# Performance work log

Measured on AMD Instinct MI355X. Metric: run time of the kernel, lower is better.

## Reference

```python
import jax, jax.numpy as jnp
import numpy as np

D = 1024
H = 16
T = D // H  # head dim; attention() scales by sqrt(Q.size(2)) == sqrt(T)
B = 4
S = 2048


def setup_inputs() -> dict:
    key = jax.random.key(0)
    ks = jax.random.split(key, 11)
    lim = 1.0 / np.sqrt(D)  # nn.Linear default init range
    inp = {
        "Q": jax.random.normal(ks[0], (B, S, D), jnp.float32),
        "K": jax.random.normal(ks[1], (B, S, D), jnp.float32),
        "V": jax.random.normal(ks[2], (B, S, D), jnp.float32),
        # per-head Q/K/V projections, stacked: weight [h, t, d], bias [h, t]
        "Wq": jax.random.uniform(ks[3], (H, T, D), jnp.float32, -lim, lim),
        "bq": jax.random.uniform(ks[4], (H, T), jnp.float32, -lim, lim),
        "Wk": jax.random.uniform(ks[5], (H, T, D), jnp.float32, -lim, lim),
        "bk": jax.random.uniform(ks[6], (H, T), jnp.float32, -lim, lim),
        "Wv": jax.random.uniform(ks[7], (H, T, D), jnp.float32, -lim, lim),
        "bv": jax.random.uniform(ks[8], (H, T), jnp.float32, -lim, lim),
        # output projection d -> d
        "Wo": jax.random.uniform(ks[9], (D, D), jnp.float32, -lim, lim),
        "bo": jax.random.uniform(ks[10], (D,), jnp.float32, -lim, lim),
    }
    return inp


def reference(Q, K, V, Wq, bq, Wk, bk, Wv, bv, Wo, bo):
    # Per-head projections, batched over heads: [b, h, s, t]
    q = jnp.einsum("bsd,htd->bhst", Q, Wq) + bq[None, :, None, :]
    k = jnp.einsum("bsd,htd->bhst", K, Wk) + bk[None, :, None, :]
    v = jnp.einsum("bsd,htd->bhst", V, Wv) + bv[None, :, None, :]
    # scaled dot-product attention; scale uses head dim T (Q.size(2) in source)
    scores = jnp.einsum("bhqt,bhkt->bhqk", q, k) / jnp.sqrt(jnp.asarray(T, q.dtype))
    probs = jax.nn.softmax(scores, axis=-1)
    ctx = jnp.einsum("bhqk,bhkt->bhqt", probs, v)
    # concat heads along feature dim (head i -> slice [i*t:(i+1)*t])
    z = ctx.transpose(0, 2, 1, 3).reshape(B, S, D)
    return jnp.einsum("bsd,ed->bse", z, Wo) + bo
```

## Files before the change

### kernel.cpp

```cpp
#include <hip/hip_runtime.h>

typedef unsigned short u16;
typedef unsigned int u32;
typedef __bf16 bf16x8 __attribute__((ext_vector_type(8)));
typedef __bf16 bf16x2 __attribute__((ext_vector_type(2)));
typedef float f32x4 __attribute__((ext_vector_type(4)));
typedef float f32x16 __attribute__((ext_vector_type(16)));
typedef unsigned int u32x2v __attribute__((ext_vector_type(2)));

#define BB 4
#define SS 2048
#define DD 1024
#define HH 16
#define TT 64

#define QSCALE 0.18033688011112042f

__device__ __forceinline__ u16 f32_to_bf16(float f) {
    unsigned int u = __float_as_uint(f);
    u += 0x7fffu + ((u >> 16) & 1u);
    return (u16)(u >> 16);
}

__device__ __forceinline__ u32 pack_bf16x2(float a, float b) {
    bf16x2 t;
    t[0] = (__bf16)a;
    t[1] = (__bf16)b;
    return __builtin_bit_cast(u32, t);
}

__device__ __forceinline__ void pswap(u32& x, u32& y) {
#if __has_builtin(__builtin_amdgcn_permlane32_swap)
    u32x2v r = __builtin_amdgcn_permlane32_swap(x, y, false, false);
    x = r[0];
    y = r[1];
#else
    u32 sx = __shfl_xor(y, 32);
    u32 sy = __shfl_xor(x, 32);
    bool lo = (threadIdx.x & 32) == 0;
    u32 nx = lo ? x : sx;
    u32 ny = lo ? sy : y;
    x = nx;
    y = ny;
#endif
}

#define GLDS(g, l) __builtin_amdgcn_global_load_lds(                              \
    (const __attribute__((address_space(1))) void*)(g),                            \
    (__attribute__((address_space(3))) void*)(l), 16, 0, 0)

struct PackArgs {
    const float* s[4];
    u16* d[4];
};

__global__ __launch_bounds__(256) void pack_multi(PackArgs a) {
    const float* __restrict__ src = a.s[blockIdx.y];
    u16* __restrict__ dst = a.d[blockIdx.y];
    int i = (blockIdx.x * 256 + threadIdx.x) * 8;
    float4 x = *(const float4*)(src + i);
    float4 y = *(const float4*)(src + i + 4);
    ushort4 o0, o1;
    o0.x = f32_to_bf16(x.x); o0.y = f32_to_bf16(x.y);
    o0.z = f32_to_bf16(x.z); o0.w = f32_to_bf16(x.w);
    o1.x = f32_to_bf16(y.x); o1.y = f32_to_bf16(y.y);
    o1.z = f32_to_bf16(y.z); o1.w = f32_to_bf16(y.w);
    *(ushort4*)(dst + i)     = o0;
    *(ushort4*)(dst + i + 4) = o1;
}

#define GEMM_CORE(Aptr, Wptr, BM, BN)                                              \
    __shared__ u16 lds_a[128 * 64];                                                \
    __shared__ u16 lds_b[128 * 64];                                                \
    const int tid = threadIdx.x;                                                   \
    const int w = tid >> 6, l = tid & 63;                                          \
    const int bm = (BM);                                                           \
    const int bn = (BN);                                                           \
    const int wm = (w >> 1) * 64;                                                  \
    const int wn = (w & 1) * 64;                                                   \
    const int srow = l >> 3;                                                       \
    const int scol = (l & 7) * 16;                                                 \
    f32x4 acc[4][4] = {};                                                          \
    const char* Abase = (const char*)(Aptr) + (size_t)bm * 2048;                   \
    const char* Bbase = (const char*)(Wptr) + (size_t)bn * 2048;                   \
    for (int kt = 0; kt < 1024; kt += 64) {                                        \
        _Pragma("unroll")                                                          \
        for (int j = 0; j < 4; ++j) {                                              \
            int chunk = w * 4 + j;                                                 \
            int r = chunk * 8 + srow;                                              \
            int csrc = scol ^ ((r & 7) << 4);                                      \
            GLDS(Abase + (size_t)r * 2048 + kt * 2 + csrc, &lds_a[chunk * 512]);   \
            GLDS(Bbase + (size_t)r * 2048 + kt * 2 + csrc, &lds_b[chunk * 512]);   \
        }                                                                          \
        __syncthreads();                                                           \
        _Pragma("unroll")                                                          \
        for (int ks = 0; ks < 2; ++ks) {                                           \
            bf16x8 af[4], bfr[4];                                                  \
            _Pragma("unroll")                                                      \
            for (int i = 0; i < 4; ++i) {                                          \
                int ra = wm + i * 16 + (l & 15);                                   \
                int ba = (ks * 64 + ((l >> 4) << 4)) ^ ((ra & 7) << 4);            \
                af[i] = *(const bf16x8*)((const char*)lds_a + ra * 128 + ba);      \
                int rb = wn + i * 16 + (l & 15);                                   \
                int bb2 = (ks * 64 + ((l >> 4) << 4)) ^ ((rb & 7) << 4);           \
                bfr[i] = *(const bf16x8*)((const char*)lds_b + rb * 128 + bb2);    \
            }                                                                      \
            _Pragma("unroll")                                                      \
            for (int mi = 0; mi < 4; ++mi)                                         \
                _Pragma("unroll")                                                  \
                for (int ni = 0; ni < 4; ++ni)                                     \
                    acc[mi][ni] = __builtin_amdgcn_mfma_f32_16x16x32_bf16(         \
                        af[mi], bfr[ni], acc[mi][ni], 0, 0, 0);                    \
        }                                                                          \
        __syncthreads();                                                           \
    }

#define XCD_SWZ(BMT, BNT)                                                          \
    const int lin_ = blockIdx.x + 8 * blockIdx.y;                                  \
    const int BMT = (lin_ & 7) * 8 + ((lin_ >> 3) >> 3);                           \
    const int BNT = (lin_ >> 3) & 7;

struct QkvArgs {
    const u16* A[3];
    const u16* W[3];
    const float* bias[3];
    u16* out[3];
};

__global__ __launch_bounds__(256, 2) void gemm_qkv(QkvArgs args) {
    const int mode = blockIdx.z;
    const u16* A = args.A[mode];
    const u16* Wp = args.W[mode];
    const float* bias = args.bias[mode];
    u16* Cb = args.out[mode];

    XCD_SWZ(bmt, bnt)
    GEMM_CORE(A, Wp, bmt * 128, bnt * 128)

    const int mq = (l >> 4) << 2;
    const float scale = (mode == 0) ? QSCALE : 1.0f;
#pragma unroll
    for (int mi = 0; mi < 4; ++mi) {
#pragma unroll
        for (int ni = 0; ni < 4; ++ni) {
            int m0 = bm + wm + mi * 16 + mq;
            int n  = bn + wn + ni * 16 + (l & 15);
            float bv = bias[n];
            f32x4 v = acc[mi][ni];
            int hh = n >> 6, t = n & 63;
            if (mode == 2) {
                int b = m0 >> 11, s2 = m0 & 2047;
                size_t idx = (size_t)(b * 16 + hh) * 131072
                           + (s2 >> 6) * 4096 + (t >> 5) * 2048
                           + ((s2 & 63) >> 3) * 256 + (t & 31) * 8 + (s2 & 7);
                uint2 pk2;
                pk2.x = pack_bf16x2(v[0] + bv, v[1] + bv);
                pk2.y = pack_bf16x2(v[2] + bv, v[3] + bv);
                *(uint2*)(&Cb[idx]) = pk2;
            } else {
#pragma unroll
                for (int r = 0; r < 4; ++r) {
                    int m = m0 + r;
                    int b = m >> 11, s2 = m & 2047;
                    size_t idx = (size_t)(b * 16 + hh) * 131072
                               + (s2 >> 6) * 4096 + ((s2 >> 5) & 1) * 2048
                               + (t >> 3) * 256 + (s2 & 31) * 8 + (t & 7);
                    Cb[idx] = f32_to_bf16((v[r] + bv) * scale);
                }
            }
        }
    }
}

__global__ __launch_bounds__(256, 2) void gemm_out(
    const u16* __restrict__ A, const u16* __restrict__ Wp,
    const float* __restrict__ bias, float* __restrict__ Cf)
{
    XCD_SWZ(bmt, bnt)
    GEMM_CORE(A, Wp, bmt * 128, bnt * 128)

    const int mq = (l >> 4) << 2;
#pragma unroll
    for (int mi = 0; mi < 4; ++mi) {
#pragma unroll
        for (int ni = 0; ni < 4; ++ni) {
            int m0 = bm + wm + mi * 16 + mq;
            int n  = bn + wn + ni * 16 + (l & 15);
            float bv = bias[n];
            f32x4 v = acc[mi][ni];
#pragma unroll
            for (int r = 0; r < 4; ++r)
                Cf[(size_t)(m0 + r) * 1024 + n] = v[r] + bv;
        }
    }
}

union PbU {
    u32 d[4];
    bf16x8 v;
};

__global__ __launch_bounds__(512, 4) void attn_kernel(
    const u16* __restrict__ qh,
    const u16* __restrict__ kh,
    const u16* __restrict__ vt,
    u16* __restrict__ z)
{
    __shared__ u16 k_lds[2][64 * 64];
    __shared__ u16 v_lds[2][64 * 64];
    const int tid = threadIdx.x;
    const int w = tid >> 6, l = tid & 63;
    const int l31 = l & 31, h2 = l >> 5;
    const int qb = blockIdx.x;
    const int bh = blockIdx.y;
    const size_t hb2 = (size_t)bh * 262144;

    const int qrow = qb * 256 + w * 32 + l31;
    bf16x8 qf[4];
    {
        const char* qp = (const char*)qh + hb2
                       + (size_t)(qb * 4 + (w >> 1)) * 8192
                       + (w & 1) * 4096 + (h2 << 9) + (l31 << 4);
#pragma unroll
        for (int ks = 0; ks < 4; ++ks)
            qf[ks] = *(const bf16x8*)(qp + ks * 1024);
    }

    f32x16 ctx0 = {}, ctx1 = {};
    float lsum = 0.f;

    const int dofs = w * 512;
    const char* kp = (const char*)kh + hb2 + (size_t)tid * 16;
    const char* vp = (const char*)vt + hb2 + (size_t)tid * 16;
    u16* kdst[2] = { &k_lds[0][dofs], &k_lds[1][dofs] };
    u16* vdst[2] = { &v_lds[0][dofs], &v_lds[1][dofs] };

#define ASTAGE(NB)                                                                 \
    do {                                                                           \
        GLDS(kp, kdst[NB]);                                                        \
        GLDS(vp, vdst[NB]);                                                        \
        kp += 8192; vp += 8192;                                                    \
    } while (0)

    ASTAGE(0);
    __syncthreads();

#define ABODY(CB, NB, PF)                                                          \
    {                                                                              \
        if (PF) ASTAGE(NB);                                                        \
        f32x16 sfr0 = {}, sfr1 = {};                                               \
        __builtin_amdgcn_s_setprio(1);                                             \
        _Pragma("unroll")                                                          \
        for (int ks = 0; ks < 4; ++ks) {                                           \
            int co = (ks << 10) + (h2 << 9) + (l31 << 4);    \
            const char* kb0 = (const char*)k_lds[CB] + co;                         \
            bf16x8 kf0 = *(const bf16x8*)(kb0);                                    \
            bf16x8 kf1 = *(const bf16x8*)(kb0 + 4096);                             \
            sfr0 = __builtin_amdgcn_mfma_f32_32x32x16_bf16(kf0, qf[ks], sfr0, 0, 0, 0); \
            sfr1 = __builtin_amdgcn_mfma_f32_32x32x16_bf16(kf1, qf[ks], sfr1, 0, 0, 0); \
        }                                                                          \
        __builtin_amdgcn_s_setprio(0);                                             \
            \
        uint2 Qd0[4], Qd1[4];                                                      \
        float psum = 0.f;                                                          \
        _Pragma("unroll")                                                          \
        for (int m = 0; m < 4; ++m) {                                              \
            float a0 = __builtin_amdgcn_exp2f(sfr0[4 * m + 0]);                    \
            float a1 = __builtin_amdgcn_exp2f(sfr0[4 * m + 1]);                    \
            float a2 = __builtin_amdgcn_exp2f(sfr0[4 * m + 2]);                    \
            float a3 = __builtin_amdgcn_exp2f(sfr0[4 * m + 3]);                    \
            float b0 = __builtin_amdgcn_exp2f(sfr1[4 * m + 0]);                    \
            float b1 = __builtin_amdgcn_exp2f(sfr1[4 * m + 1]);                    \
            float b2 = __builtin_amdgcn_exp2f(sfr1[4 * m + 2]);                    \
            float b3 = __builtin_amdgcn_exp2f(sfr1[4 * m + 3]);                    \
            psum += ((a0 + a1) + (a2 + a3)) + ((b0 + b1) + (b2 + b3));             \
            Qd0[m] = make_uint2(pack_bf16x2(a0, a1), pack_bf16x2(a2, a3));         \
            Qd1[m] = make_uint2(pack_bf16x2(b0, b1), pack_bf16x2(b2, b3));         \
        }                                                                          \
        lsum += psum;                                                              \
                         \
        __builtin_amdgcn_s_setprio(1);                                             \
        _Pragma("unroll")                                                          \
        for (int ks = 0; ks < 4; ++ks) {                                           \
            u32 x0, x1, y0, y1;                                                    \
            if (ks == 0) { x0 = Qd0[0].x; x1 = Qd0[0].y; y0 = Qd0[1].x; y1 = Qd0[1].y; } \
            else if (ks == 1) { x0 = Qd0[2].x; x1 = Qd0[2].y; y0 = Qd0[3].x; y1 = Qd0[3].y; } \
            else if (ks == 2) { x0 = Qd1[0].x; x1 = Qd1[0].y; y0 = Qd1[1].x; y1 = Qd1[1].y; } \
            else { x0 = Qd1[2].x; x1 = Qd1[2].y; y0 = Qd1[3].x; y1 = Qd1[3].y; }   \
            pswap(x0, y0);                                                         \
            pswap(x1, y1);                                                         \
            PbU pu;                                                                \
            pu.d[0] = x0; pu.d[1] = x1; pu.d[2] = y0; pu.d[3] = y1;                \
            int co = (ks << 10) + (h2 << 9) + (l31 << 4);                          \
            const char* vb0 = (const char*)v_lds[CB] + co;                         \
            bf16x8 vf0 = *(const bf16x8*)(vb0);                                    \
            bf16x8 vf1 = *(const bf16x8*)(vb0 + 4096);                             \
            ctx0 = __builtin_amdgcn_mfma_f32_32x32x16_bf16(vf0, pu.v, ctx0, 0, 0, 0); \
            ctx1 = __builtin_amdgcn_mfma_f32_32x32x16_bf16(vf1, pu.v, ctx1, 0, 0, 0); \
        }                                                                          \
        __builtin_amdgcn_s_setprio(0);                                             \
        __syncthreads();                                                           \
    }

    for (int tt = 0; tt < 32; tt += 2) {
        ABODY(0, 1, true)
        ABODY(1, 0, (tt < 30))
    }
#undef ABODY
#undef ASTAGE

    float rsum = lsum + __shfl_xor(lsum, 32);
    float rinv = 1.0f / rsum;

    const int b = bh >> 4, hd = bh & 15;
    u16* zrow = z + ((size_t)(b * 2048 + qrow)) * 1024 + hd * 64 + (h2 << 2);
#pragma unroll
    for (int m = 0; m < 4; ++m) {
        ushort4 o0, o1;
        o0.x = f32_to_bf16(ctx0[4 * m + 0] * rinv);
        o0.y = f32_to_bf16(ctx0[4 * m + 1] * rinv);
        o0.z = f32_to_bf16(ctx0[4 * m + 2] * rinv);
        o0.w = f32_to_bf16(ctx0[4 * m + 3] * rinv);
        o1.x = f32_to_bf16(ctx1[4 * m + 0] * rinv);
        o1.y = f32_to_bf16(ctx1[4 * m + 1] * rinv);
        o1.z = f32_to_bf16(ctx1[4 * m + 2] * rinv);
        o1.w = f32_to_bf16(ctx1[4 * m + 3] * rinv);
        *(ushort4*)(zrow + 8 * m)      = o0;
        *(ushort4*)(zrow + 8 * m + 32) = o1;
    }
}

extern "C" void kernel_launch(void* const* d_in, const int* in_sizes, int n_in,
                              void* d_out, int out_size, void* d_ws, size_t ws_size,
                              hipStream_t stream) {
    const float* Q  = (const float*)d_in[0];
    const float* K  = (const float*)d_in[1];
    const float* V  = (const float*)d_in[2];
    const float* Wq = (const float*)d_in[3];
    const float* bq = (const float*)d_in[4];
    const float* Wk = (const float*)d_in[5];
    const float* bk = (const float*)d_in[6];
    const float* Wv = (const float*)d_in[7];
    const float* bv = (const float*)d_in[8];
    const float* Wo = (const float*)d_in[9];
    const float* bo = (const float*)d_in[10];

    const int ACT = BB * SS * DD;
    const int WEL = DD * DD;

    u16* ws  = (u16*)d_ws;
    u16* Qb  = ws;
    u16* Kb  = Qb + ACT;
    u16* Vb  = Kb + ACT;
    u16* Wqb = Vb + ACT;
    u16* Wkb = Wqb + WEL;
    u16* Wvb = Wkb + WEL;
    u16* Wob = Wvb + WEL;
    u16* qhb = Wob + WEL;
    u16* khb = qhb + ACT;
    u16* vtb = khb + ACT;
    u16* zb  = vtb + ACT;

    PackArgs pa;
    pa.s[0] = Q;  pa.s[1] = K;  pa.s[2] = V;  pa.s[3] = nullptr;
    pa.d[0] = Qb; pa.d[1] = Kb; pa.d[2] = Vb; pa.d[3] = nullptr;
    pack_multi<<<dim3(ACT / 2048, 3), 256, 0, stream>>>(pa);

    PackArgs pb;
    pb.s[0] = Wq;  pb.s[1] = Wk;  pb.s[2] = Wv;  pb.s[3] = Wo;
    pb.d[0] = Wqb; pb.d[1] = Wkb; pb.d[2] = Wvb; pb.d[3] = Wob;
    pack_multi<<<dim3(WEL / 2048, 4), 256, 0, stream>>>(pb);

    QkvArgs qa;
    qa.A[0] = Qb;  qa.A[1] = Kb;  qa.A[2] = Vb;
    qa.W[0] = Wqb; qa.W[1] = Wkb; qa.W[2] = Wvb;
    qa.bias[0] = bq; qa.bias[1] = bk; qa.bias[2] = bv;
    qa.out[0] = qhb; qa.out[1] = khb; qa.out[2] = vtb;
    gemm_qkv<<<dim3(8, 64, 3), 256, 0, stream>>>(qa);

    attn_kernel<<<dim3(8, 64), 512, 0, stream>>>(qhb, khb, vtb, zb);

    gemm_out<<<dim3(8, 64), 256, 0, stream>>>(zb, Wob, bo, (float*)d_out);
}
```

Measured before the change: 191.2 us.

## Double attention KV tile size per barrier and merge pack launches into one

The attention kernel now stages 128 keys/values per pipeline stage instead of 64, processing two 64-key halves between each __syncthreads. This halves the number of barriers and prefetch rounds over the sequence, at the cost of doubling LDS use (64 KB per block), which may lower occupancy. Separately, the two fp32-to-bf16 pack launches are fused into a single 1D launch that maps block IDs to seven tensors, removing one kernel launch.

```diff
diff --git a/kernel.cpp b/kernel.cpp
--- a/kernel.cpp
+++ b/kernel.cpp
@@ -49,15 +49,19 @@
     (const __attribute__((address_space(1))) void*)(g),                            \
     (__attribute__((address_space(3))) void*)(l), 16, 0, 0)
 
-struct PackArgs {
-    const float* s[4];
-    u16* d[4];
+struct PackArgs7 {
+    const float* s[7];
+    u16* d[7];
 };
 
-__global__ __launch_bounds__(256) void pack_multi(PackArgs a) {
-    const float* __restrict__ src = a.s[blockIdx.y];
-    u16* __restrict__ dst = a.d[blockIdx.y];
-    int i = (blockIdx.x * 256 + threadIdx.x) * 8;
+__global__ __launch_bounds__(256) void pack_multi(PackArgs7 a) {
+    int bid = blockIdx.x;
+    int t, off;
+    if (bid < 12288) { t = bid >> 12;            off = bid & 4095; }
+    else             { int r = bid - 12288; t = 3 + (r >> 9); off = r & 511; }
+    const float* __restrict__ src = a.s[t];
+    u16* __restrict__ dst = a.d[t];
+    int i = (off * 256 + threadIdx.x) * 8;
     float4 x = *(const float4*)(src + i);
     float4 y = *(const float4*)(src + i + 4);
     ushort4 o0, o1;
@@ -206,8 +210,8 @@
     const u16* __restrict__ vt,
     u16* __restrict__ z)
 {
-    __shared__ u16 k_lds[2][64 * 64];
-    __shared__ u16 v_lds[2][64 * 64];
+    __shared__ u16 k_lds[2][128 * 64];
+    __shared__ u16 v_lds[2][128 * 64];
     const int tid = threadIdx.x;
     const int w = tid >> 6, l = tid & 63;
     const int l31 = l & 31, h2 = l >> 5;
@@ -237,22 +241,21 @@
 
 #define ASTAGE(NB)                                                                 \
     do {                                                                           \
-        GLDS(kp, kdst[NB]);                                                        \
-        GLDS(vp, vdst[NB]);                                                        \
-        kp += 8192; vp += 8192;                                                    \
+        GLDS(kp, kdst[NB]);          GLDS(kp + 8192, kdst[NB] + 4096);             \
+        GLDS(vp, vdst[NB]);          GLDS(vp + 8192, vdst[NB] + 4096);             \
+        kp += 16384; vp += 16384;                                                  \
     } while (0)
 
     ASTAGE(0);
     __syncthreads();
 
-#define ABODY(CB, NB, PF)                                                          \
+#define AHALF(CB, HF)                                                              \
     {                                                                              \
-        if (PF) ASTAGE(NB);                                                        \
         f32x16 sfr0 = {}, sfr1 = {};                                               \
         __builtin_amdgcn_s_setprio(1);                                             \
         _Pragma("unroll")                                                          \
         for (int ks = 0; ks < 4; ++ks) {                                           \
-            int co = (ks << 10) + (h2 << 9) + (l31 << 4);    \
+            int co = (HF) * 8192 + (ks << 10) + (h2 << 9) + (l31 << 4);            \
             const char* kb0 = (const char*)k_lds[CB] + co;                         \
             bf16x8 kf0 = *(const bf16x8*)(kb0);                                    \
             bf16x8 kf1 = *(const bf16x8*)(kb0 + 4096);                             \
@@ -260,7 +263,6 @@
             sfr1 = __builtin_amdgcn_mfma_f32_32x32x16_bf16(kf1, qf[ks], sfr1, 0, 0, 0); \
         }                                                                          \
         __builtin_amdgcn_s_setprio(0);                                             \
-            \
         uint2 Qd0[4], Qd1[4];                                                      \
         float psum = 0.f;                                                          \
         _Pragma("unroll")                                                          \
@@ -278,7 +280,6 @@
             Qd1[m] = make_uint2(pack_bf16x2(b0, b1), pack_bf16x2(b2, b3));         \
         }                                                                          \
         lsum += psum;                                                              \
-                         \
         __builtin_amdgcn_s_setprio(1);                                             \
         _Pragma("unroll")                                                          \
         for (int ks = 0; ks < 4; ++ks) {                                           \
@@ -291,7 +292,7 @@
             pswap(x1, y1);                                                         \
             PbU pu;                                                                \
             pu.d[0] = x0; pu.d[1] = x1; pu.d[2] = y0; pu.d[3] = y1;                \
-            int co = (ks << 10) + (h2 << 9) + (l31 << 4);                          \
+            int co = (HF) * 8192 + (ks << 10) + (h2 << 9) + (l31 << 4);            \
             const char* vb0 = (const char*)v_lds[CB] + co;                         \
             bf16x8 vf0 = *(const bf16x8*)(vb0);                                    \
             bf16x8 vf1 = *(const bf16x8*)(vb0 + 4096);                             \
@@ -299,14 +300,22 @@
             ctx1 = __builtin_amdgcn_mfma_f32_32x32x16_bf16(vf1, pu.v, ctx1, 0, 0, 0); \
         }                                                                          \
         __builtin_amdgcn_s_setprio(0);                                             \
+    }
+
+#define ABODY(CB, NB, PF)                                                          \
+    {                                                                              \
+        if (PF) ASTAGE(NB);                                                        \
+        AHALF(CB, 0)                                                               \
+        AHALF(CB, 1)                                                               \
         __syncthreads();                                                           \
     }
 
-    for (int tt = 0; tt < 32; tt += 2) {
+    for (int tt = 0; tt < 16; tt += 2) {
         ABODY(0, 1, true)
-        ABODY(1, 0, (tt < 30))
+        ABODY(1, 0, (tt < 14))
     }
 #undef ABODY
+#undef AHALF
 #undef ASTAGE
 
     float rsum = lsum + __shfl_xor(lsum, 32);
@@ -361,15 +370,12 @@
     u16* vtb = khb + ACT;
     u16* zb  = vtb + ACT;
 
-    PackArgs pa;
-    pa.s[0] = Q;  pa.s[1] = K;  pa.s[2] = V;  pa.s[3] = nullptr;
-    pa.d[0] = Qb; pa.d[1] = Kb; pa.d[2] = Vb; pa.d[3] = nullptr;
-    pack_multi<<<dim3(ACT / 2048, 3), 256, 0, stream>>>(pa);
-
-    PackArgs pb;
-    pb.s[0] = Wq;  pb.s[1] = Wk;  pb.s[2] = Wv;  pb.s[3] = Wo;
-    pb.d[0] = Wqb; pb.d[1] = Wkb; pb.d[2] = Wvb; pb.d[3] = Wob;
-    pack_multi<<<dim3(WEL / 2048, 4), 256, 0, stream>>>(pb);
+    PackArgs7 pk;
+    pk.s[0] = Q;  pk.s[1] = K;  pk.s[2] = V;
+    pk.s[3] = Wq; pk.s[4] = Wk; pk.s[5] = Wv; pk.s[6] = Wo;
+    pk.d[0] = Qb;  pk.d[1] = Kb;  pk.d[2] = Vb;
+    pk.d[3] = Wqb; pk.d[4] = Wkb; pk.d[5] = Wvb; pk.d[6] = Wob;
+    pack_multi<<<dim3(14336), 256, 0, stream>>>(pk);
 
     QkvArgs qa;
     qa.A[0] = Qb;  qa.A[1] = Kb;  qa.A[2] = Vb;
```

Result: slower. 390.6 us (+104.3%).
